# Kernel tuning notes

Hardware: AMD Instinct MI355X
Metric: run time of the kernel (lower is better)

Reference implementation:

```python
import jax, jax.numpy as jnp
import numpy as np

B, IN, H, MID = 16384, 256, 512, 64
GRID_SIZE, ORDER = 5, 3
GRID_LO, GRID_HI = -1.0, 1.0
NB = GRID_SIZE + ORDER  # 8 spline basis functions per input feature
LN_EPS = 1e-5


def make_grid(in_features):
    h = (GRID_HI - GRID_LO) / GRID_SIZE
    g = np.arange(-ORDER, GRID_SIZE + ORDER + 1, dtype=np.float32) * h + GRID_LO
    return jnp.asarray(np.tile(g, (in_features, 1)))  # (in, grid_size + 2*order + 1)


def layer_norm(x, g, b):
    mu = jnp.mean(x, axis=-1, keepdims=True)
    var = jnp.var(x, axis=-1, keepdims=True)
    return (x - mu) * jax.lax.rsqrt(var + LN_EPS) * g + b


def b_splines(x, grid):
    # x: (B, in), grid: (in, G). Cox-de Boor recursion (efficient-kan convention).
    xe = x[:, :, None]
    bases = ((xe >= grid[:, :-1]) & (xe < grid[:, 1:])).astype(x.dtype)
    for k in range(1, ORDER + 1):
        left = (xe - grid[:, :-(k + 1)]) / (grid[:, k:-1] - grid[:, :-(k + 1)])
        right = (grid[:, k + 1:] - xe) / (grid[:, k + 1:] - grid[:, 1:-k])
        bases = left * bases[:, :, :-1] + right * bases[:, :, 1:]
    return bases  # (B, in, NB)


def kan_linear(x, base_w, spline_w, scaler, grid):
    # base path: silu(x) @ W_base^T ; spline path: B-spline bases contracted with scaled spline weights
    base = jax.nn.silu(x) @ base_w.T
    bs = b_splines(x, grid)
    spline = jnp.einsum('bik,oik->bo', bs, spline_w * scaler[:, :, None])
    return base + spline


def setup_inputs() -> dict:
    key = jax.random.key(0)
    ks = jax.random.split(key, 24)

    def n(k, shape, fan_in):
        return jax.random.normal(k, shape, dtype=jnp.float32) / np.sqrt(fan_in)

    H2 = 2 * H
    return {
        'x': jax.random.normal(ks[0], (B, IN), jnp.float32),
        'h_prev': jax.random.normal(ks[1], (B, H), jnp.float32),
        'ip_w': n(ks[2], (H, IN), IN), 'ip_b': jnp.zeros((H,), jnp.float32),
        'rg_w': n(ks[3], (H, H2), H2), 'rg_b': jnp.zeros((H,), jnp.float32),
        'rg_g': jnp.ones((H,), jnp.float32), 'rg_beta': jnp.zeros((H,), jnp.float32),
        'ug_w': n(ks[4], (H, H2), H2), 'ug_b': jnp.zeros((H,), jnp.float32),
        'ug_g': jnp.ones((H,), jnp.float32), 'ug_beta': jnp.zeros((H,), jnp.float32),
        'k1_base': n(ks[5], (MID, H2), H2),
        'k1_spline': n(ks[6], (MID, H2, NB), H2) * 0.1,
        'k1_scaler': n(ks[7], (MID, H2), H2) + 1.0,
        'grid1': make_grid(H2),
        'k2_base': n(ks[8], (H, MID), MID),
        'k2_spline': n(ks[9], (H, MID, NB), MID) * 0.1,
        'k2_scaler': n(ks[10], (H, MID), MID) + 1.0,
        'grid2': make_grid(MID),
        'cn_g': jnp.ones((H,), jnp.float32), 'cn_b': jnp.zeros((H,), jnp.float32),
        'rp_w': n(ks[11], (H, H2), H2), 'rp_b': jnp.zeros((H,), jnp.float32),
    }


def reference(x, h_prev, ip_w, ip_b, rg_w, rg_b, rg_g, rg_beta, ug_w, ug_b, ug_g, ug_beta,
              k1_base, k1_spline, k1_scaler, grid1, k2_base, k2_spline, k2_scaler, grid2,
              cn_g, cn_b, rp_w, rp_b):
    x_proj = x @ ip_w.T + ip_b
    combined = jnp.concatenate([x_proj, h_prev], axis=1)  # (B, 2H)
    # reset gate is computed in the original forward but never used; kept for faithfulness
    reset = jnp.tanh(layer_norm(combined @ rg_w.T + rg_b, rg_g, rg_beta))  # noqa: F841
    update = jax.nn.sigmoid(layer_norm(combined @ ug_w.T + ug_b, ug_g, ug_beta))
    # KAN candidate: [2H] -> 64 -> H
    mid = kan_linear(combined, k1_base, k1_spline, k1_scaler, grid1)
    h_cand = kan_linear(mid, k2_base, k2_spline, k2_scaler, grid2)
    residual = combined @ rp_w.T + rp_b
    h_cand = layer_norm(h_cand + residual, cn_g, cn_b)
    h_cand = layer_norm(h_cand, cn_g, cn_b)  # same LayerNorm applied twice, as in source
    h_cand = jax.nn.silu(h_cand)
    h_t = (1.0 - update) * h_prev + update * h_cand
    return h_t
```

## Files before the change

kernel.cpp:

```cpp
#include <hip/hip_runtime.h>
#include <hip/hip_bf16.h>

#define BATCH 16384

typedef __attribute__((ext_vector_type(8))) short short8;
typedef __attribute__((ext_vector_type(4))) float f32x4;

typedef const __attribute__((address_space(1))) uint* gas_t;
typedef __attribute__((address_space(3))) uint* las_t;

__device__ __forceinline__ void gl_lds16(const void* g, void* l) {
    __builtin_amdgcn_global_load_lds((gas_t)g, (las_t)l, 16, 0, 0);
}

__device__ __forceinline__ float bf2f(uint u) { union { uint u; float f; } v; v.u = u << 16; return v.f; }
__device__ __forceinline__ ushort f2bf(float f) {
    union { float f; uint u; } v; v.f = f;
    uint r = v.u + 0x7fffu + ((v.u >> 16) & 1u);
    return (ushort)(r >> 16);
}
__device__ __forceinline__ uint pack2(float a, float b) { return (uint)f2bf(a) | ((uint)f2bf(b) << 16); }
__device__ __forceinline__ uint pack_trunc(float lo, float hi) {
    return __builtin_amdgcn_perm(__float_as_uint(hi), __float_as_uint(lo), 0x07060302u);
}
__device__ __forceinline__ float sigmoidf_(float x) { return __builtin_amdgcn_rcpf(1.0f + __expf(-x)); }
__device__ __forceinline__ float siluf_(float x)    { return x * sigmoidf_(x); }

__device__ __forceinline__ void xcd_swz(int& bm, int& bn) {
    int lin = blockIdx.x + blockIdx.y * 128;
    int c = lin & 7, s = lin >> 3;
    bm = c * 16 + (s >> 2);
    bn = s & 3;
}

__device__ __forceinline__ void bases_packed(float x, float g0, float inv_h, uint o[4]) {
    float u = (x - g0) * inv_h;
    float fl = floorf(u);
    float f = u - fl;
    float f2 = f * f, f3 = f2 * f;
    float Ca = f3 * (1.0f / 6.0f);
    float Cb = (1.0f / 6.0f) + 0.5f * (f + f2 - f3);
    float Cc = (2.0f / 3.0f) + 0.5f * f3 - f2;
    float Cd = (1.0f / 6.0f) + 0.5f * (f2 - f) - f3 * (1.0f / 6.0f);
    int t0 = (int)fl;
    t0 = max(-8, min(t0, 19));
    uint dlo = pack_trunc(Cd, Cc);
    uint dhi = pack_trunc(Cb, Ca);
    unsigned long long D = (unsigned long long)dlo | ((unsigned long long)dhi << 32);
    int sp = t0 * 16 - 48;
    unsigned long long l1 = D << (sp & 63);
    unsigned long long r1 = D >> ((-sp) & 63);
    unsigned long long r2 = D >> ((64 - sp) & 63);
    unsigned long long l2 = D << ((sp - 64) & 63);
    unsigned long long lo = (sp >= 0) ? (sp < 64 ? l1 : 0ull) : (sp > -64 ? r1 : 0ull);
    unsigned long long hi = (sp > 0 && sp < 128) ? (sp < 64 ? r2 : l2) : 0ull;
    o[0] = (uint)lo; o[1] = (uint)(lo >> 32); o[2] = (uint)hi; o[3] = (uint)(hi >> 32);
}

__global__ __launch_bounds__(256) void prep_all(const float* __restrict__ hp,
                                                const float* __restrict__ ip_w, const float* __restrict__ ug_w,
                                                const float* __restrict__ rp,  const float* __restrict__ k2b,
                                                const float* __restrict__ k2s, const float* __restrict__ k2sc,
                                                const float* __restrict__ k1b, const float* __restrict__ k1s,
                                                const float* __restrict__ k1sc,
                                                ushort* __restrict__ acat,
                                                ushort* __restrict__ ipw, ushort* __restrict__ ugw,
                                                ushort* __restrict__ wcat, ushort* __restrict__ w1aug) {
    int t = blockIdx.x * 256 + threadIdx.x;
    if (t < 1048576) {
        int b = t >> 6, j = (t & 63) * 8;
        const float4* s = (const float4*)(hp + (size_t)b * 512 + j);
        float4 a = s[0], c = s[1];
        uint4 o; o.x = pack2(a.x, a.y); o.y = pack2(a.z, a.w); o.z = pack2(c.x, c.y); o.w = pack2(c.z, c.w);
        *(uint4*)(acat + (size_t)b * 1600 + 512 + j) = o;
        return;
    }
    t -= 1048576;
    if (t < 131072) { ipw[t] = f2bf(ip_w[t]); return; }
    t -= 131072;
    if (t < 524288) { ugw[t] = f2bf(ug_w[t]); return; }
    t -= 524288;
    if (t < 819200) {
        int n = t / 1600, c = t % 1600; float v;
        if (c < 1024) v = rp[n * 1024 + c];
        else if (c < 1088) v = k2b[n * 64 + (c - 1024)];
        else { int i = (c - 1088) >> 3, k = (c - 1088) & 7; v = k2s[(n * 64 + i) * 8 + k] * k2sc[n * 64 + i]; }
        wcat[t] = f2bf(v); return;
    }
    t -= 819200;
    if (t < 589824) {
        int n = t / 9216, c = t % 9216; float v;
        if (c < 1024) v = k1b[n * 1024 + c];
        else { int i = (c - 1024) >> 3, k = (c - 1024) & 7; v = k1s[(n * 1024 + i) * 8 + k] * k1sc[n * 1024 + i]; }
        w1aug[t] = f2bf(v);
    }
}

__global__ __launch_bounds__(256) void gemm_mfma(const ushort* __restrict__ A, int lda,
                                                 const ushort* __restrict__ Wt, int ldw,
                                                 const float* __restrict__ bias,
                                                 ushort* __restrict__ C, int ldc, int K) {
    __shared__ ushort As[2][128 * 64];
    __shared__ ushort Bs[2][128 * 64];
    const int tid = threadIdx.x;
    const int w = tid >> 6, lane = tid & 63;
    const int fr = lane & 15, fq = lane >> 4;
    int bm, bn; xcd_swz(bm, bn);
    const int m0 = bm * 128, n0 = bn * 128;
    const int wm = w & 1, wn = w >> 1;

    const int srow8 = lane >> 3;
    const int scol  = ((lane & 7) ^ srow8) << 3;
    const ushort* gA[4]; const ushort* gB[4]; int fa[4];
#pragma unroll
    for (int j = 0; j < 4; ++j) {
        int rowj = (j * 4 + w) * 8 + srow8;
        fa[j] = (j * 4 + w) * 512 + lane * 8;
        gA[j] = A  + (size_t)(m0 + rowj) * lda + scol;
        gB[j] = Wt + (size_t)(n0 + rowj) * ldw + scol;
    }
    const int nt = K / 64;
#pragma unroll
    for (int j = 0; j < 4; ++j) {
        gl_lds16(gA[j], &As[0][fa[j]]); gl_lds16(gB[j], &Bs[0][fa[j]]);
        gA[j] += 64; gB[j] += 64;
    }
    f32x4 acc[4][4] = {};
    int cur = 0;
    for (int t = 0; t < nt; ++t) {
        __syncthreads();
        if (t + 1 < nt) {
#pragma unroll
            for (int j = 0; j < 4; ++j) {
                gl_lds16(gA[j], &As[cur ^ 1][fa[j]]); gl_lds16(gB[j], &Bs[cur ^ 1][fa[j]]);
                gA[j] += 64; gB[j] += 64;
            }
        }
#pragma unroll
        for (int s = 0; s < 2; ++s) {
            const int csw = ((s * 4 + fq) ^ (fr & 7)) << 3;
            short8 af[4], bv[4];
#pragma unroll
            for (int mi = 0; mi < 4; ++mi)
                af[mi] = *(const short8*)(&As[cur][(wm * 64 + mi * 16 + fr) * 64 + csw]);
#pragma unroll
            for (int ni = 0; ni < 4; ++ni)
                bv[ni] = *(const short8*)(&Bs[cur][(wn * 64 + ni * 16 + fr) * 64 + csw]);
#pragma unroll
            for (int mi = 0; mi < 4; ++mi)
#pragma unroll
                for (int ni = 0; ni < 4; ++ni)
                    acc[mi][ni] = __builtin_amdgcn_mfma_f32_16x16x32_bf16(af[mi], bv[ni], acc[mi][ni], 0, 0, 0);
        }
        cur ^= 1;
    }
#pragma unroll
    for (int mi = 0; mi < 4; ++mi) {
#pragma unroll
        for (int ni = 0; ni < 4; ++ni) {
            int n = n0 + wn * 64 + ni * 16 + fr;
            float bvs = bias[n];
#pragma unroll
            for (int r = 0; r < 4; ++r) {
                int m = m0 + wm * 64 + mi * 16 + fq * 4 + r;
                C[(size_t)m * ldc + n] = f2bf(acc[mi][ni][r] + bvs);
            }
        }
    }
}

__global__ __launch_bounds__(256) void gemm_ip(const float* __restrict__ X,
                                               const ushort* __restrict__ Wt,
                                               const float* __restrict__ bias,
                                               ushort* __restrict__ acat) {
    __shared__ ushort As[2][128 * 64];
    __shared__ ushort Bs[2][128 * 64];
    const int tid = threadIdx.x;
    const int w = tid >> 6, lane = tid & 63;
    const int fr = lane & 15, fq = lane >> 4;
    int bm, bn; xcd_swz(bm, bn);
    const int m0 = bm * 128, n0 = bn * 128;
    const int wm = w & 1, wn = w >> 1;

    const int srow8 = lane >> 3;
    const int scol = ((lane & 7) ^ srow8) << 3;
    const ushort* gB[4]; int fa[4];
#pragma unroll
    for (int j = 0; j < 4; ++j) {
        int rowj = (j * 4 + w) * 8 + srow8;
        fa[j] = (j * 4 + w) * 512 + lane * 8;
        gB[j] = Wt + (size_t)(n0 + rowj) * 256 + scol;
    }
    const float* gA[4]; int ar[4];
#pragma unroll
    for (int j = 0; j < 4; ++j) {
        int rj = j * 32 + (tid >> 3);
        int lc = (tid & 7) ^ (rj & 7);
        ar[j] = rj * 64 + (tid & 7) * 8;
        gA[j] = X + (size_t)(m0 + rj) * 256 + lc * 8;
    }
    float4 va[4], vb[4];
#pragma unroll
    for (int j = 0; j < 4; ++j) { gl_lds16(gB[j], &Bs[0][fa[j]]); gB[j] += 64; }
#pragma unroll
    for (int j = 0; j < 4; ++j) { va[j] = *(const float4*)gA[j]; vb[j] = *(const float4*)(gA[j] + 4); gA[j] += 64; }
#pragma unroll
    for (int j = 0; j < 4; ++j) {
        uint4 o; o.x = pack2(va[j].x, va[j].y); o.y = pack2(va[j].z, va[j].w);
        o.z = pack2(vb[j].x, vb[j].y); o.w = pack2(vb[j].z, vb[j].w);
        *(uint4*)&As[0][ar[j]] = o;
    }
    f32x4 acc[4][4] = {};
    int cur = 0;
    for (int t = 0; t < 4; ++t) {
        __syncthreads();
        if (t < 3) {
#pragma unroll
            for (int j = 0; j < 4; ++j) { gl_lds16(gB[j], &Bs[cur ^ 1][fa[j]]); gB[j] += 64; }
#pragma unroll
            for (int j = 0; j < 4; ++j) { va[j] = *(const float4*)gA[j]; vb[j] = *(const float4*)(gA[j] + 4); gA[j] += 64; }
        }
#pragma unroll
        for (int s = 0; s < 2; ++s) {
            const int csw = ((s * 4 + fq) ^ (fr & 7)) << 3;
            short8 af[4], bv[4];
#pragma unroll
            for (int mi = 0; mi < 4; ++mi)
                af[mi] = *(const short8*)(&As[cur][(wm * 64 + mi * 16 + fr) * 64 + csw]);
#pragma unroll
            for (int ni = 0; ni < 4; ++ni)
                bv[ni] = *(const short8*)(&Bs[cur][(wn * 64 + ni * 16 + fr) * 64 + csw]);
#pragma unroll
            for (int mi = 0; mi < 4; ++mi)
#pragma unroll
                for (int ni = 0; ni < 4; ++ni)
                    acc[mi][ni] = __builtin_amdgcn_mfma_f32_16x16x32_bf16(af[mi], bv[ni], acc[mi][ni], 0, 0, 0);
        }
        if (t < 3) {
#pragma unroll
            for (int j = 0; j < 4; ++j) {
                uint4 o; o.x = pack2(va[j].x, va[j].y); o.y = pack2(va[j].z, va[j].w);
                o.z = pack2(vb[j].x, vb[j].y); o.w = pack2(vb[j].z, vb[j].w);
                *(uint4*)&As[cur ^ 1][ar[j]] = o;
            }
        }
        cur ^= 1;
    }
#pragma unroll
    for (int mi = 0; mi < 4; ++mi) {
#pragma unroll
        for (int ni = 0; ni < 4; ++ni) {
            int n = n0 + wn * 64 + ni * 16 + fr;
            float bvs = bias[n];
#pragma unroll
            for (int r = 0; r < 4; ++r) {
                int m = m0 + wm * 64 + mi * 16 + fq * 4 + r;
                acat[(size_t)m * 1600 + n] = f2bf(acc[mi][ni][r] + bvs);
            }
        }
    }
}

__global__ __launch_bounds__(256) void kan1_mfma(const ushort* __restrict__ acat,
                                                 const ushort* __restrict__ w1aug,
                                                 const float* __restrict__ grid1,
                                                 float* __restrict__ midp) {
    __shared__ ushort As[2][64 * 64];
    __shared__ ushort Bs[2][64 * 64];
    const int tid = threadIdx.x;
    const int w = tid >> 6, lane = tid & 63;
    const int fr = lane & 15, fq = lane >> 4;
    const int m0 = blockIdx.x * 64;
    const int kb = blockIdx.y;
    const float g0 = grid1[0];
    const float inv_h = 1.0f / (grid1[1] - g0);

    const int srow = tid >> 3, sc = tid & 7;
    const int xr = srow & 7;
    const int lc8 = (sc ^ xr) << 3;
    const ushort* wB0  = w1aug + (size_t)srow * 9216 + lc8;
    const ushort* wB1  = w1aug + (size_t)(srow + 32) * 9216 + lc8;
    const int wpo = srow * 64 + lc8;
    const int wm = w & 1, wn = w >> 1;
    const int cB = kb * 128;
    const int bB = 1024 + kb * 1024;

    const ushort* aR0 = acat + (size_t)(m0 + srow) * 1600;
    const ushort* aR1 = acat + (size_t)(m0 + srow + 32) * 1600;

    uint4 sA0[2], sA1[2];
#pragma unroll
    for (int s = 0; s < 2; ++s) {
        sA0[s] = *(const uint4*)(aR0 + cB + s * 64 + sc * 8);
        sA1[s] = *(const uint4*)(aR1 + cB + s * 64 + sc * 8);
    }
    uint xa[16], xb[16];
#pragma unroll
    for (int bs = 0; bs < 16; ++bs) {
        xa[bs] = aR0[cB + bs * 8 + sc];
        xb[bs] = aR1[cB + bs * 8 + sc];
    }

    f32x4 acc[2][2] = {};
    auto stageB = [&](int c, int buf) {
        gl_lds16(wB0 + c, &Bs[buf][tid * 8]);
        gl_lds16(wB1 + c, &Bs[buf][2048 + tid * 8]);
    };
    auto stageAsilu = [&](int s, int buf) {
        uint r0[4] = {sA0[s].x, sA0[s].y, sA0[s].z, sA0[s].w};
        uint r1[4] = {sA1[s].x, sA1[s].y, sA1[s].z, sA1[s].w};
        uint o0[4], o1[4];
#pragma unroll
        for (int p = 0; p < 4; ++p) {
            o0[p] = pack_trunc(siluf_(bf2f(r0[p] & 0xffffu)), siluf_(bf2f(r0[p] >> 16)));
            o1[p] = pack_trunc(siluf_(bf2f(r1[p] & 0xffffu)), siluf_(bf2f(r1[p] >> 16)));
        }
        uint4 q0; q0.x = o0[0]; q0.y = o0[1]; q0.z = o0[2]; q0.w = o0[3];
        uint4 q1; q1.x = o1[0]; q1.y = o1[1]; q1.z = o1[2]; q1.w = o1[3];
        *(uint4*)&As[buf][wpo] = q0;
        *(uint4*)&As[buf][2048 + wpo] = q1;
    };
    auto stageAbases = [&](uint x0u, uint x1u, int buf) {
        uint o0[4], o1[4];
        bases_packed(bf2f(x0u), g0, inv_h, o0);
        bases_packed(bf2f(x1u), g0, inv_h, o1);
        uint4 q0; q0.x = o0[0]; q0.y = o0[1]; q0.z = o0[2]; q0.w = o0[3];
        uint4 q1; q1.x = o1[0]; q1.y = o1[1]; q1.z = o1[2]; q1.w = o1[3];
        *(uint4*)&As[buf][wpo] = q0;
        *(uint4*)&As[buf][2048 + wpo] = q1;
    };
    auto mfma_step = [&](int buf) {
        __builtin_amdgcn_s_setprio(1);
#pragma unroll
        for (int s2 = 0; s2 < 2; ++s2) {
            short8 af[2], bv[2];
#pragma unroll
            for (int mi = 0; mi < 2; ++mi) {
                int arow = wm * 32 + mi * 16 + fr;
                af[mi] = *(const short8*)(&As[buf][arow * 64 + (((s2 * 4 + fq) ^ (arow & 7)) << 3)]);
            }
#pragma unroll
            for (int ni = 0; ni < 2; ++ni) {
                int brow = wn * 32 + ni * 16 + fr;
                bv[ni] = *(const short8*)(&Bs[buf][brow * 64 + (((s2 * 4 + fq) ^ (brow & 7)) << 3)]);
            }
#pragma unroll
            for (int mi = 0; mi < 2; ++mi)
#pragma unroll
                for (int ni = 0; ni < 2; ++ni)
                    acc[mi][ni] = __builtin_amdgcn_mfma_f32_16x16x32_bf16(af[mi], bv[ni], acc[mi][ni], 0, 0, 0);
        }
        __builtin_amdgcn_s_setprio(0);
    };

    stageB(cB, 0); stageAsilu(0, 0);
    __syncthreads();
    stageB(cB + 64, 1); stageAsilu(1, 1);
    mfma_step(0);
    __syncthreads();
    stageB(bB, 0); stageAbases(xa[0], xb[0], 0);
    mfma_step(1);
#pragma unroll
    for (int bs = 0; bs < 15; ++bs) {
        __syncthreads();
        stageB(bB + (bs + 1) * 64, (bs + 1) & 1);
        stageAbases(xa[bs + 1], xb[bs + 1], (bs + 1) & 1);
        mfma_step(bs & 1);
    }
    __syncthreads();
    mfma_step(1);

    float* outp = midp + (size_t)kb * (BATCH * 64);
#pragma unroll
    for (int mi = 0; mi < 2; ++mi)
#pragma unroll
        for (int ni = 0; ni < 2; ++ni)
#pragma unroll
            for (int r = 0; r < 4; ++r)
                outp[(size_t)(m0 + wm * 32 + mi * 16 + fq * 4 + r) * 64 + wn * 32 + ni * 16 + fr] = acc[mi][ni][r];
}

__global__ __launch_bounds__(256) void bs2_kernel(const float* __restrict__ midp,
                                                  const float* __restrict__ grid2,
                                                  ushort* __restrict__ acat) {
    int t4 = blockIdx.x * 256 + threadIdx.x;
    if (t4 >= BATCH * 16) return;
    int base = t4 * 4;
    float4 x4 = {0.f, 0.f, 0.f, 0.f};
#pragma unroll
    for (int p = 0; p < 8; ++p) {
        float4 v = *(const float4*)(midp + (size_t)p * (BATCH * 64) + base);
        x4.x += v.x; x4.y += v.y; x4.z += v.z; x4.w += v.w;
    }
    int b = base >> 6, i = base & 63;
    float g0 = grid2[0], inv_h = 1.0f / (grid2[1] - g0);
    float xs[4] = {x4.x, x4.y, x4.z, x4.w};
    uint2 sil;
    sil.x = pack2(siluf_(xs[0]), siluf_(xs[1]));
    sil.y = pack2(siluf_(xs[2]), siluf_(xs[3]));
    *(uint2*)&acat[(size_t)b * 1600 + 1024 + i] = sil;
#pragma unroll
    for (int e = 0; e < 4; ++e) {
        uint o[4];
        bases_packed(xs[e], g0, inv_h, o);
        uint4 o4; o4.x = o[0]; o4.y = o[1]; o4.z = o[2]; o4.w = o[3];
        *(uint4*)&acat[(size_t)b * 1600 + 1088 + (i + e) * 8] = o4;
    }
}

__device__ __forceinline__ void block_reduce_2(float& a, float& b, float (*red)[4]) {
#pragma unroll
    for (int off = 32; off; off >>= 1) {
        a += __shfl_xor(a, off, 64);
        b += __shfl_xor(b, off, 64);
    }
    int lane = threadIdx.x & 63, wid = threadIdx.x >> 6;
    if (lane == 0) { red[0][wid] = a; red[1][wid] = b; }
    __syncthreads();
    a = red[0][0] + red[0][1] + red[0][2] + red[0][3];
    b = red[1][0] + red[1][1] + red[1][2] + red[1][3];
}

__global__ __launch_bounds__(256) void final2(const ushort* __restrict__ ug,
                                              const ushort* __restrict__ hcb,
                                              const ushort* __restrict__ acat,
                                              const float* __restrict__ ug_g,
                                              const float* __restrict__ ug_beta,
                                              const float* __restrict__ cg,
                                              const float* __restrict__ cb,
                                              float* __restrict__ out) {
    int row = blockIdx.x, tid = threadIdx.x;
    __shared__ float rA[2][4], rB[2][4], rC[2][4];
    float u0 = bf2f((uint)ug[(size_t)row * 512 + tid]);
    float u1 = bf2f((uint)ug[(size_t)row * 512 + tid + 256]);
    float h0 = bf2f((uint)hcb[(size_t)row * 512 + tid]);
    float h1 = bf2f((uint)hcb[(size_t)row * 512 + tid + 256]);
    float hp0 = bf2f((uint)acat[(size_t)row * 1600 + 512 + tid]);
    float hp1 = bf2f((uint)acat[(size_t)row * 1600 + 768 + tid]);
    float s = u0 + u1, ss = u0 * u0 + u1 * u1;
    block_reduce_2(s, ss, rA);
    float mu = s * (1.0f / 512.0f);
    float var = ss * (1.0f / 512.0f) - mu * mu;
    float r = rsqrtf(var + 1e-5f);
    float uu0 = sigmoidf_((u0 - mu) * r * ug_g[tid] + ug_beta[tid]);
    float uu1 = sigmoidf_((u1 - mu) * r * ug_g[tid + 256] + ug_beta[tid + 256]);
    float cg0 = cg[tid], cg1 = cg[tid + 256], cb0 = cb[tid], cb1 = cb[tid + 256];
    float s2 = h0 + h1, ss2 = h0 * h0 + h1 * h1;
    block_reduce_2(s2, ss2, rB);
    float mu2 = s2 * (1.0f / 512.0f);
    float var2 = ss2 * (1.0f / 512.0f) - mu2 * mu2;
    float r2 = rsqrtf(var2 + 1e-5f);
    float w0 = (h0 - mu2) * r2 * cg0 + cb0;
    float w1 = (h1 - mu2) * r2 * cg1 + cb1;
    float s3 = w0 + w1, ss3 = w0 * w0 + w1 * w1;
    block_reduce_2(s3, ss3, rC);
    float mu3 = s3 * (1.0f / 512.0f);
    float var3 = ss3 * (1.0f / 512.0f) - mu3 * mu3;
    float r3 = rsqrtf(var3 + 1e-5f);
    float c0 = siluf_((w0 - mu3) * r3 * cg0 + cb0);
    float c1 = siluf_((w1 - mu3) * r3 * cg1 + cb1);
    size_t o0 = (size_t)row * 512 + tid, o1 = o0 + 256;
    out[o0] = (1.0f - uu0) * hp0 + uu0 * c0;
    out[o1] = (1.0f - uu1) * hp1 + uu1 * c1;
}

extern "C" void kernel_launch(void* const* d_in, const int* in_sizes, int n_in,
                              void* d_out, int out_size, void* d_ws, size_t ws_size,
                              hipStream_t stream) {
    const float* x        = (const float*)d_in[0];
    const float* h_prev   = (const float*)d_in[1];
    const float* ip_w     = (const float*)d_in[2];
    const float* ip_b     = (const float*)d_in[3];
    const float* ug_w     = (const float*)d_in[8];
    const float* ug_b     = (const float*)d_in[9];
    const float* ug_g     = (const float*)d_in[10];
    const float* ug_beta  = (const float*)d_in[11];
    const float* k1_base  = (const float*)d_in[12];
    const float* k1_spline= (const float*)d_in[13];
    const float* k1_scaler= (const float*)d_in[14];
    const float* grid1    = (const float*)d_in[15];
    const float* k2_base  = (const float*)d_in[16];
    const float* k2_spline= (const float*)d_in[17];
    const float* k2_scaler= (const float*)d_in[18];
    const float* grid2    = (const float*)d_in[19];
    const float* cn_g     = (const float*)d_in[20];
    const float* cn_b     = (const float*)d_in[21];
    const float* rp_w     = (const float*)d_in[22];
    const float* rp_b     = (const float*)d_in[23];
    float* out = (float*)d_out;
    char* W = (char*)d_ws;

    ushort* Acat    = (ushort*)(W);
    ushort* ug_bf   = (ushort*)(W + 52428800);
    float*  midp    = (float*) (W + 69206016);
    ushort* hc_bf   = (ushort*)(W + 102760448);
    ushort* ipw_bf  = (ushort*)(W + 136314880);
    ushort* ugw_bf  = (ushort*)(W + 136577024);
    ushort* wcat    = (ushort*)(W + 137625600);
    ushort* w1aug   = (ushort*)(W + 139264000);

    hipLaunchKernelGGL(prep_all, dim3(12160), dim3(256), 0, stream,
                       h_prev, ip_w, ug_w, rp_w, k2_base, k2_spline, k2_scaler,
                       k1_base, k1_spline, k1_scaler,
                       Acat, ipw_bf, ugw_bf, wcat, w1aug);

    hipLaunchKernelGGL(gemm_ip, dim3(BATCH / 128, 4), dim3(256), 0, stream,
                       x, ipw_bf, ip_b, Acat);

    hipLaunchKernelGGL(gemm_mfma, dim3(BATCH / 128, 4), dim3(256), 0, stream,
                       Acat, 1600, ugw_bf, 1024, ug_b, ug_bf, 512, 1024);

    hipLaunchKernelGGL(kan1_mfma, dim3(BATCH / 64, 8), dim3(256), 0, stream,
                       Acat, w1aug, grid1, midp);
    hipLaunchKernelGGL(bs2_kernel, dim3(BATCH * 16 / 256), dim3(256), 0, stream, midp, grid2, Acat);

    hipLaunchKernelGGL(gemm_mfma, dim3(BATCH / 128, 4), dim3(256), 0, stream,
                       Acat, 1600, wcat, 1600, rp_b, hc_bf, 512, 1600);

    hipLaunchKernelGGL(final2, dim3(BATCH), dim3(256), 0, stream, ug_bf, hc_bf, Acat, ug_g, ug_beta, cn_g, cn_b, out);
}
```

Measured before the change: 161.5 us.

## Fuse input projection into prep kernel and merge update-gate GEMM with spline bases

The input-projection GEMM now runs inside the prep kernel, converting the fp32 ip_w to bf16 on the fly. Conversion of h_prev and the other weights shares that launch, so the separate ipw conversion goes away. The update-gate GEMM is merged with the layer-2 B-spline basis kernel into one launch, interleaving GEMM blocks with elementwise blocks, and the kan1 partial sums are stored as bf16 instead of fp32. The aim is fewer launches, better overlap between independent work, and less intermediate traffic. In exchange, the partial sums lose precision and the heterogeneous blocks may balance poorly or have lower occupancy because of their shared-memory footprint.

```diff
diff --git a/kernel.cpp b/kernel.cpp
--- a/kernel.cpp
+++ b/kernel.cpp
@@ -57,42 +57,122 @@
     o[0] = (uint)lo; o[1] = (uint)(lo >> 32); o[2] = (uint)hi; o[3] = (uint)(hi >> 32);
 }
 
-__global__ __launch_bounds__(256) void prep_all(const float* __restrict__ hp,
-                                                const float* __restrict__ ip_w, const float* __restrict__ ug_w,
-                                                const float* __restrict__ rp,  const float* __restrict__ k2b,
-                                                const float* __restrict__ k2s, const float* __restrict__ k2sc,
-                                                const float* __restrict__ k1b, const float* __restrict__ k1s,
-                                                const float* __restrict__ k1sc,
-                                                ushort* __restrict__ acat,
-                                                ushort* __restrict__ ipw, ushort* __restrict__ ugw,
-                                                ushort* __restrict__ wcat, ushort* __restrict__ w1aug) {
-    int t = blockIdx.x * 256 + threadIdx.x;
-    if (t < 1048576) {
-        int b = t >> 6, j = (t & 63) * 8;
-        const float4* s = (const float4*)(hp + (size_t)b * 512 + j);
-        float4 a = s[0], c = s[1];
-        uint4 o; o.x = pack2(a.x, a.y); o.y = pack2(a.z, a.w); o.z = pack2(c.x, c.y); o.w = pack2(c.z, c.w);
-        *(uint4*)(acat + (size_t)b * 1600 + 512 + j) = o;
+__global__ __launch_bounds__(256) void ip_prep(const float* __restrict__ X,
+                                               const float* __restrict__ ip_w, const float* __restrict__ ip_b,
+                                               const float* __restrict__ hp, const float* __restrict__ ug_w,
+                                               const float* __restrict__ rp,  const float* __restrict__ k2b,
+                                               const float* __restrict__ k2s, const float* __restrict__ k2sc,
+                                               const float* __restrict__ k1b, const float* __restrict__ k1s,
+                                               const float* __restrict__ k1sc,
+                                               ushort* __restrict__ acat, ushort* __restrict__ ugw,
+                                               ushort* __restrict__ wcat, ushort* __restrict__ w1aug) {
+    __shared__ ushort As[2][128 * 64];
+    __shared__ ushort Bs[2][128 * 64];
+    const int tid = threadIdx.x;
+    if (blockIdx.x < 512) {
+        const int w = tid >> 6, lane = tid & 63;
+        const int fr = lane & 15, fq = lane >> 4;
+        const int uid = blockIdx.x;
+        const int m0 = (uid & 127) * 128, n0 = (uid >> 7) * 128;
+        const int wm = w & 1, wn = w >> 1;
+
+        const float* gA[4]; const float* gBf[4]; int ar[4];
+#pragma unroll
+        for (int j = 0; j < 4; ++j) {
+            int rj = j * 32 + (tid >> 3);
+            int lc = (tid & 7) ^ (rj & 7);
+            ar[j] = rj * 64 + (tid & 7) * 8;
+            gA[j]  = X    + (size_t)(m0 + rj) * 256 + lc * 8;
+            gBf[j] = ip_w + (size_t)(n0 + rj) * 256 + lc * 8;
+        }
+        float4 va[4], vb[4], wa[4], wb[4];
+        auto ldnext = [&]() {
+#pragma unroll
+            for (int j = 0; j < 4; ++j) {
+                va[j] = *(const float4*)gA[j];  vb[j] = *(const float4*)(gA[j] + 4);  gA[j] += 64;
+                wa[j] = *(const float4*)gBf[j]; wb[j] = *(const float4*)(gBf[j] + 4); gBf[j] += 64;
+            }
+        };
+        auto wrbuf = [&](int buf) {
+#pragma unroll
+            for (int j = 0; j < 4; ++j) {
+                uint4 o; o.x = pack2(va[j].x, va[j].y); o.y = pack2(va[j].z, va[j].w);
+                o.z = pack2(vb[j].x, vb[j].y); o.w = pack2(vb[j].z, vb[j].w);
+                *(uint4*)&As[buf][ar[j]] = o;
+                uint4 q; q.x = pack2(wa[j].x, wa[j].y); q.y = pack2(wa[j].z, wa[j].w);
+                q.z = pack2(wb[j].x, wb[j].y); q.w = pack2(wb[j].z, wb[j].w);
+                *(uint4*)&Bs[buf][ar[j]] = q;
+            }
+        };
+        ldnext(); wrbuf(0);
+        f32x4 acc[4][4] = {};
+        int cur = 0;
+        for (int t = 0; t < 4; ++t) {
+            __syncthreads();
+            if (t < 3) ldnext();
+#pragma unroll
+            for (int s = 0; s < 2; ++s) {
+                const int csw = ((s * 4 + fq) ^ (fr & 7)) << 3;
+                short8 af[4], bv[4];
+#pragma unroll
+                for (int mi = 0; mi < 4; ++mi)
+                    af[mi] = *(const short8*)(&As[cur][(wm * 64 + mi * 16 + fr) * 64 + csw]);
+#pragma unroll
+                for (int ni = 0; ni < 4; ++ni)
+                    bv[ni] = *(const short8*)(&Bs[cur][(wn * 64 + ni * 16 + fr) * 64 + csw]);
+#pragma unroll
+                for (int mi = 0; mi < 4; ++mi)
+#pragma unroll
+                    for (int ni = 0; ni < 4; ++ni)
+                        acc[mi][ni] = __builtin_amdgcn_mfma_f32_16x16x32_bf16(af[mi], bv[ni], acc[mi][ni], 0, 0, 0);
+            }
+            if (t < 3) wrbuf(cur ^ 1);
+            cur ^= 1;
+        }
+#pragma unroll
+        for (int mi = 0; mi < 4; ++mi) {
+#pragma unroll
+            for (int ni = 0; ni < 4; ++ni) {
+                int n = n0 + wn * 64 + ni * 16 + fr;
+                float bvs = ip_b[n];
+#pragma unroll
+                for (int r = 0; r < 4; ++r) {
+                    int m = m0 + wm * 64 + mi * 16 + fq * 4 + r;
+                    acat[(size_t)m * 1600 + n] = f2bf(acc[mi][ni][r] + bvs);
+                }
+            }
+        }
         return;
     }
-    t -= 1048576;
-    if (t < 131072) { ipw[t] = f2bf(ip_w[t]); return; }
-    t -= 131072;
-    if (t < 524288) { ugw[t] = f2bf(ug_w[t]); return; }
-    t -= 524288;
-    if (t < 819200) {
-        int n = t / 1600, c = t % 1600; float v;
-        if (c < 1024) v = rp[n * 1024 + c];
-        else if (c < 1088) v = k2b[n * 64 + (c - 1024)];
-        else { int i = (c - 1088) >> 3, k = (c - 1088) & 7; v = k2s[(n * 64 + i) * 8 + k] * k2sc[n * 64 + i]; }
-        wcat[t] = f2bf(v); return;
-    }
-    t -= 819200;
-    if (t < 589824) {
-        int n = t / 9216, c = t % 9216; float v;
-        if (c < 1024) v = k1b[n * 1024 + c];
-        else { int i = (c - 1024) >> 3, k = (c - 1024) & 7; v = k1s[(n * 1024 + i) * 8 + k] * k1sc[n * 1024 + i]; }
-        w1aug[t] = f2bf(v);
+    const int t00 = (blockIdx.x - 512) * 256 + tid;
+#pragma unroll
+    for (int rep = 0; rep < 4; ++rep) {
+        int t = t00 + rep * 745472;
+        if (t < 1048576) {
+            int b = t >> 6, j = (t & 63) * 8;
+            const float4* s = (const float4*)(hp + (size_t)b * 512 + j);
+            float4 a = s[0], c = s[1];
+            uint4 o; o.x = pack2(a.x, a.y); o.y = pack2(a.z, a.w); o.z = pack2(c.x, c.y); o.w = pack2(c.z, c.w);
+            *(uint4*)(acat + (size_t)b * 1600 + 512 + j) = o;
+            continue;
+        }
+        t -= 1048576;
+        if (t < 524288) { ugw[t] = f2bf(ug_w[t]); continue; }
+        t -= 524288;
+        if (t < 819200) {
+            int n = t / 1600, c = t % 1600; float v;
+            if (c < 1024) v = rp[n * 1024 + c];
+            else if (c < 1088) v = k2b[n * 64 + (c - 1024)];
+            else { int i = (c - 1088) >> 3, k = (c - 1088) & 7; v = k2s[(n * 64 + i) * 8 + k] * k2sc[n * 64 + i]; }
+            wcat[t] = f2bf(v); continue;
+        }
+        t -= 819200;
+        if (t < 589824) {
+            int n = t / 9216, c = t % 9216; float v;
+            if (c < 1024) v = k1b[n * 1024 + c];
+            else { int i = (c - 1024) >> 3, k = (c - 1024) & 7; v = k1s[(n * 1024 + i) * 8 + k] * k1sc[n * 1024 + i]; }
+            w1aug[t] = f2bf(v);
+        }
     }
 }
 
@@ -169,102 +249,10 @@
     }
 }
 
-__global__ __launch_bounds__(256) void gemm_ip(const float* __restrict__ X,
-                                               const ushort* __restrict__ Wt,
-                                               const float* __restrict__ bias,
-                                               ushort* __restrict__ acat) {
-    __shared__ ushort As[2][128 * 64];
-    __shared__ ushort Bs[2][128 * 64];
-    const int tid = threadIdx.x;
-    const int w = tid >> 6, lane = tid & 63;
-    const int fr = lane & 15, fq = lane >> 4;
-    int bm, bn; xcd_swz(bm, bn);
-    const int m0 = bm * 128, n0 = bn * 128;
-    const int wm = w & 1, wn = w >> 1;
-
-    const int srow8 = lane >> 3;
-    const int scol = ((lane & 7) ^ srow8) << 3;
-    const ushort* gB[4]; int fa[4];
-#pragma unroll
-    for (int j = 0; j < 4; ++j) {
-        int rowj = (j * 4 + w) * 8 + srow8;
-        fa[j] = (j * 4 + w) * 512 + lane * 8;
-        gB[j] = Wt + (size_t)(n0 + rowj) * 256 + scol;
-    }
-    const float* gA[4]; int ar[4];
-#pragma unroll
-    for (int j = 0; j < 4; ++j) {
-        int rj = j * 32 + (tid >> 3);
-        int lc = (tid & 7) ^ (rj & 7);
-        ar[j] = rj * 64 + (tid & 7) * 8;
-        gA[j] = X + (size_t)(m0 + rj) * 256 + lc * 8;
-    }
-    float4 va[4], vb[4];
-#pragma unroll
-    for (int j = 0; j < 4; ++j) { gl_lds16(gB[j], &Bs[0][fa[j]]); gB[j] += 64; }
-#pragma unroll
-    for (int j = 0; j < 4; ++j) { va[j] = *(const float4*)gA[j]; vb[j] = *(const float4*)(gA[j] + 4); gA[j] += 64; }
-#pragma unroll
-    for (int j = 0; j < 4; ++j) {
-        uint4 o; o.x = pack2(va[j].x, va[j].y); o.y = pack2(va[j].z, va[j].w);
-        o.z = pack2(vb[j].x, vb[j].y); o.w = pack2(vb[j].z, vb[j].w);
-        *(uint4*)&As[0][ar[j]] = o;
-    }
-    f32x4 acc[4][4] = {};
-    int cur = 0;
-    for (int t = 0; t < 4; ++t) {
-        __syncthreads();
-        if (t < 3) {
-#pragma unroll
-            for (int j = 0; j < 4; ++j) { gl_lds16(gB[j], &Bs[cur ^ 1][fa[j]]); gB[j] += 64; }
-#pragma unroll
-            for (int j = 0; j < 4; ++j) { va[j] = *(const float4*)gA[j]; vb[j] = *(const float4*)(gA[j] + 4); gA[j] += 64; }
-        }
-#pragma unroll
-        for (int s = 0; s < 2; ++s) {
-            const int csw = ((s * 4 + fq) ^ (fr & 7)) << 3;
-            short8 af[4], bv[4];
-#pragma unroll
-            for (int mi = 0; mi < 4; ++mi)
-                af[mi] = *(const short8*)(&As[cur][(wm * 64 + mi * 16 + fr) * 64 + csw]);
-#pragma unroll
-            for (int ni = 0; ni < 4; ++ni)
-                bv[ni] = *(const short8*)(&Bs[cur][(wn * 64 + ni * 16 + fr) * 64 + csw]);
-#pragma unroll
-            for (int mi = 0; mi < 4; ++mi)
-#pragma unroll
-                for (int ni = 0; ni < 4; ++ni)
-                    acc[mi][ni] = __builtin_amdgcn_mfma_f32_16x16x32_bf16(af[mi], bv[ni], acc[mi][ni], 0, 0, 0);
-        }
-        if (t < 3) {
-#pragma unroll
-            for (int j = 0; j < 4; ++j) {
-                uint4 o; o.x = pack2(va[j].x, va[j].y); o.y = pack2(va[j].z, va[j].w);
-                o.z = pack2(vb[j].x, vb[j].y); o.w = pack2(vb[j].z, vb[j].w);
-                *(uint4*)&As[cur ^ 1][ar[j]] = o;
-            }
-        }
-        cur ^= 1;
-    }
-#pragma unroll
-    for (int mi = 0; mi < 4; ++mi) {
-#pragma unroll
-        for (int ni = 0; ni < 4; ++ni) {
-            int n = n0 + wn * 64 + ni * 16 + fr;
-            float bvs = bias[n];
-#pragma unroll
-            for (int r = 0; r < 4; ++r) {
-                int m = m0 + wm * 64 + mi * 16 + fq * 4 + r;
-                acat[(size_t)m * 1600 + n] = f2bf(acc[mi][ni][r] + bvs);
-            }
-        }
-    }
-}
-
 __global__ __launch_bounds__(256) void kan1_mfma(const ushort* __restrict__ acat,
                                                  const ushort* __restrict__ w1aug,
                                                  const float* __restrict__ grid1,
-                                                 float* __restrict__ midp) {
+                                                 ushort* __restrict__ midp) {
     __shared__ ushort As[2][64 * 64];
     __shared__ ushort Bs[2][64 * 64];
     const int tid = threadIdx.x;
@@ -370,41 +358,114 @@
     __syncthreads();
     mfma_step(1);
 
-    float* outp = midp + (size_t)kb * (BATCH * 64);
+    ushort* outp = midp + (size_t)kb * (BATCH * 64);
 #pragma unroll
     for (int mi = 0; mi < 2; ++mi)
 #pragma unroll
         for (int ni = 0; ni < 2; ++ni)
 #pragma unroll
             for (int r = 0; r < 4; ++r)
-                outp[(size_t)(m0 + wm * 32 + mi * 16 + fq * 4 + r) * 64 + wn * 32 + ni * 16 + fr] = acc[mi][ni][r];
-}
-
-__global__ __launch_bounds__(256) void bs2_kernel(const float* __restrict__ midp,
-                                                  const float* __restrict__ grid2,
-                                                  ushort* __restrict__ acat) {
-    int t4 = blockIdx.x * 256 + threadIdx.x;
-    if (t4 >= BATCH * 16) return;
-    int base = t4 * 4;
-    float4 x4 = {0.f, 0.f, 0.f, 0.f};
+                outp[(size_t)(m0 + wm * 32 + mi * 16 + fq * 4 + r) * 64 + wn * 32 + ni * 16 + fr] = f2bf(acc[mi][ni][r]);
+}
+
+__global__ __launch_bounds__(256) void ug_bs2(const ushort* __restrict__ acat,
+                                              const ushort* __restrict__ ugw,
+                                              const float* __restrict__ ug_b,
+                                              ushort* __restrict__ ug_bf,
+                                              const ushort* __restrict__ midp,
+                                              const float* __restrict__ grid2,
+                                              ushort* __restrict__ acat_w) {
+    __shared__ ushort As[2][128 * 64];
+    __shared__ ushort Bs[2][128 * 64];
+    const int tid = threadIdx.x;
+    const int lin = blockIdx.x;
+    const int g = lin / 3, r3 = lin % 3;
+    if (r3 == 0) {
+        const int w = tid >> 6, lane = tid & 63;
+        const int fr = lane & 15, fq = lane >> 4;
+        const int m0 = (g & 127) * 128, n0 = (g >> 7) * 128;
+        const int wm = w & 1, wn = w >> 1;
+        const int srow8 = lane >> 3;
+        const int scol  = ((lane & 7) ^ srow8) << 3;
+        const ushort* gA[4]; const ushort* gB[4]; int fa[4];
+#pragma unroll
+        for (int j = 0; j < 4; ++j) {
+            int rowj = (j * 4 + w) * 8 + srow8;
+            fa[j] = (j * 4 + w) * 512 + lane * 8;
+            gA[j] = acat + (size_t)(m0 + rowj) * 1600 + scol;
+            gB[j] = ugw  + (size_t)(n0 + rowj) * 1024 + scol;
+        }
+#pragma unroll
+        for (int j = 0; j < 4; ++j) {
+            gl_lds16(gA[j], &As[0][fa[j]]); gl_lds16(gB[j], &Bs[0][fa[j]]);
+            gA[j] += 64; gB[j] += 64;
+        }
+        f32x4 acc[4][4] = {};
+        int cur = 0;
+        for (int t = 0; t < 16; ++t) {
+            __syncthreads();
+            if (t + 1 < 16) {
+#pragma unroll
+                for (int j = 0; j < 4; ++j) {
+                    gl_lds16(gA[j], &As[cur ^ 1][fa[j]]); gl_lds16(gB[j], &Bs[cur ^ 1][fa[j]]);
+                    gA[j] += 64; gB[j] += 64;
+                }
+            }
+#pragma unroll
+            for (int s = 0; s < 2; ++s) {
+                const int csw = ((s * 4 + fq) ^ (fr & 7)) << 3;
+                short8 af[4], bv[4];
+#pragma unroll
+                for (int mi = 0; mi < 4; ++mi)
+                    af[mi] = *(const short8*)(&As[cur][(wm * 64 + mi * 16 + fr) * 64 + csw]);
+#pragma unroll
+                for (int ni = 0; ni < 4; ++ni)
+                    bv[ni] = *(const short8*)(&Bs[cur][(wn * 64 + ni * 16 + fr) * 64 + csw]);
+#pragma unroll
+                for (int mi = 0; mi < 4; ++mi)
+#pragma unroll
+                    for (int ni = 0; ni < 4; ++ni)
+                        acc[mi][ni] = __builtin_amdgcn_mfma_f32_16x16x32_bf16(af[mi], bv[ni], acc[mi][ni], 0, 0, 0);
+            }
+            cur ^= 1;
+        }
+#pragma unroll
+        for (int mi = 0; mi < 4; ++mi) {
+#pragma unroll
+            for (int ni = 0; ni < 4; ++ni) {
+                int n = n0 + wn * 64 + ni * 16 + fr;
+                float bvs = ug_b[n];
+#pragma unroll
+                for (int r = 0; r < 4; ++r) {
+                    int m = m0 + wm * 64 + mi * 16 + fq * 4 + r;
+                    ug_bf[(size_t)m * 512 + n] = f2bf(acc[mi][ni][r] + bvs);
+                }
+            }
+        }
+        return;
+    }
+    const int bid = g * 2 + (r3 - 1);
+    const int t4 = bid * 256 + tid;
+    const int base = t4 * 4;
+    float xs[4] = {0.f, 0.f, 0.f, 0.f};
 #pragma unroll
     for (int p = 0; p < 8; ++p) {
-        float4 v = *(const float4*)(midp + (size_t)p * (BATCH * 64) + base);
-        x4.x += v.x; x4.y += v.y; x4.z += v.z; x4.w += v.w;
-    }
-    int b = base >> 6, i = base & 63;
+        uint2 v = *(const uint2*)(midp + (size_t)p * (BATCH * 64) + base);
+        xs[0] += bf2f(v.x & 0xffffu); xs[1] += bf2f(v.x >> 16);
+        xs[2] += bf2f(v.y & 0xffffu); xs[3] += bf2f(v.y >> 16);
+    }
+    const int b = base >> 6, i = base & 63;
     float g0 = grid2[0], inv_h = 1.0f / (grid2[1] - g0);
-    float xs[4] = {x4.x, x4.y, x4.z, x4.w};
     uint2 sil;
     sil.x = pack2(siluf_(xs[0]), siluf_(xs[1]));
     sil.y = pack2(siluf_(xs[2]), siluf_(xs[3]));
-    *(uint2*)&acat[(size_t)b * 1600 + 1024 + i] = sil;
+    *(uint2*)&acat_w[(size_t)b * 1600 + 1024 + i] = sil;
 #pragma unroll
     for (int e = 0; e < 4; ++e) {
         uint o[4];
         bases_packed(xs[e], g0, inv_h, o);
         uint4 o4; o4.x = o[0]; o4.y = o[1]; o4.z = o[2]; o4.w = o[3];
-        *(uint4*)&acat[(size_t)b * 1600 + 1088 + (i + e) * 8] = o4;
+        *(uint4*)&acat_w[(size_t)b * 1600 + 1088 + (i + e) * 8] = o4;
     }
 }
 
@@ -492,27 +553,22 @@
 
     ushort* Acat    = (ushort*)(W);
     ushort* ug_bf   = (ushort*)(W + 52428800);
-    float*  midp    = (float*) (W + 69206016);
+    ushort* midp    = (ushort*)(W + 69206016);
     ushort* hc_bf   = (ushort*)(W + 102760448);
-    ushort* ipw_bf  = (ushort*)(W + 136314880);
     ushort* ugw_bf  = (ushort*)(W + 136577024);
     ushort* wcat    = (ushort*)(W + 137625600);
     ushort* w1aug   = (ushort*)(W + 139264000);
 
-    hipLaunchKernelGGL(prep_all, dim3(12160), dim3(256), 0, stream,
-                       h_prev, ip_w, ug_w, rp_w, k2_base, k2_spline, k2_scaler,
+    hipLaunchKernelGGL(ip_prep, dim3(3424), dim3(256), 0, stream,
+                       x, ip_w, ip_b, h_prev, ug_w, rp_w, k2_base, k2_spline, k2_scaler,
                        k1_base, k1_spline, k1_scaler,
-                       Acat, ipw_bf, ugw_bf, wcat, w1aug);
-
-    hipLaunchKernelGGL(gemm_ip, dim3(BATCH / 128, 4), dim3(256), 0, stream,
-                       x, ipw_bf, ip_b, Acat);
-
-    hipLaunchKernelGGL(gemm_mfma, dim3(BATCH / 128, 4), dim3(256), 0, stream,
-                       Acat, 1600, ugw_bf, 1024, ug_b, ug_bf, 512, 1024);
+                       Acat, ugw_bf, wcat, w1aug);
 
     hipLaunchKernelGGL(kan1_mfma, dim3(BATCH / 64, 8), dim3(256), 0, stream,
                        Acat, w1aug, grid1, midp);
-    hipLaunchKernelGGL(bs2_kernel, dim3(BATCH * 16 / 256), dim3(256), 0, stream, midp, grid2, Acat);
+
+    hipLaunchKernelGGL(ug_bs2, dim3(1536), dim3(256), 0, stream,
+                       Acat, ugw_bf, ug_b, ug_bf, midp, grid2, Acat);
 
     hipLaunchKernelGGL(gemm_mfma, dim3(BATCH / 128, 4), dim3(256), 0, stream,
                        Acat, 1600, wcat, 1600, rp_b, hc_bf, 512, 1600);
```

After: 173.2 us. 1.07x slower.
